# Performance work log

Hardware: AMD Instinct MI355X
Metric: run time of the kernel (lower is better)

The kernel has to match this reference:

```python
import jax, jax.numpy as jnp
import numpy as np

N_GRID = 16      # reservoir_n
CHANNELS = 4
R = 2            # receptive-field radius -> 5x5 kernel
T_STEPS = 8
NEG_SLOPE = 0.1


def _extract_patches(S):
    # S: [b, C, n, n] -> patches [b, C, 5, 5, n, n] (kernel offsets u,v)
    Sp = jnp.pad(S, ((0, 0), (0, 0), (R, R), (R, R)))
    k = 2 * R + 1
    rows = [jnp.stack([Sp[:, :, du:du + N_GRID, dv:dv + N_GRID] for dv in range(k)], axis=2)
            for du in range(k)]
    return jnp.stack(rows, axis=2)  # [b, C, k, k, n, n]


def _reservoir_step(S, W):
    # W: [n, n, C_out, C_in, k, k]; per-pixel unique weights (locally connected)
    patches = _extract_patches(S)                       # [b, c, u, v, y, x]
    out = jnp.einsum('bcuvyx,yxocuv->boyx', patches, W)  # [b, C, n, n]
    return jnp.where(out > 0, out, NEG_SLOPE * out)      # leaky_relu(0.1)


def setup_inputs() -> dict:
    key = jax.random.key(0)
    k1, k2 = jax.random.split(key)
    x = jax.random.normal(k1, (8192, 784), dtype=jnp.float32)
    # scale weights down so the T-step recurrence stays numerically tame
    W = jax.random.normal(k2, (N_GRID, N_GRID, CHANNELS, CHANNELS, 2 * R + 1, 2 * R + 1),
                          dtype=jnp.float32) * 0.05
    return {"x": x, "W": W}


def reference(x, W):
    batch = x.shape[0]
    total = N_GRID * N_GRID * CHANNELS  # 1024
    padded = jnp.pad(x, ((0, 0), (0, total - x.shape[1])))
    S = padded.reshape(batch, CHANNELS, N_GRID, N_GRID)
    for _ in range(T_STEPS):
        S = _reservoir_step(S, W)
    S_pooled = S.mean(axis=1)                 # pool over channels -> [b, n, n]
    return S_pooled.reshape(batch, -1)        # [b, n*n]
```

## Files before the change

kernel.cpp:

```cpp
#include <hip/hip_runtime.h>

#define NG 16
#define NC 4
#define BPB 8
#define TSTEPS 8
#define PITCH 34
#define CROW (NG * PITCH)

__device__ __forceinline__ void fma8(float w, const float4& s0, const float4& s1,
                                     float4& a0, float4& a1) {
    a0.x = fmaf(w, s0.x, a0.x);
    a0.y = fmaf(w, s0.y, a0.y);
    a0.z = fmaf(w, s0.z, a0.z);
    a0.w = fmaf(w, s0.w, a0.w);
    a1.x = fmaf(w, s1.x, a1.x);
    a1.y = fmaf(w, s1.y, a1.y);
    a1.z = fmaf(w, s1.z, a1.z);
    a1.w = fmaf(w, s1.w, a1.w);
}

__device__ __forceinline__ float4 lrelu4(float4 v) {
    float4 r;
    r.x = v.x > 0.f ? v.x : 0.1f * v.x;
    r.y = v.y > 0.f ? v.y : 0.1f * v.y;
    r.z = v.z > 0.f ? v.z : 0.1f * v.z;
    r.w = v.w > 0.f ? v.w : 0.1f * v.w;
    return r;
}

__global__ void wt_transpose(const float* __restrict__ W, float4* __restrict__ Wt) {
    int t = blockIdx.x * 256 + threadIdx.x;
    if (t >= 25600) return;
    int r = t >> 8;
    int pix = t & 255;
    int c = r / 25, uv = r - c * 25, u = uv / 5, v = uv - u * 5;
    int y = pix >> 4, x = pix & 15;
    float4 w = make_float4(0.f, 0.f, 0.f, 0.f);
    if ((unsigned)(y + u - 2) < 16u && (unsigned)(x + v - 2) < 16u) {
        int base = pix * 400 + c * 25 + uv;
        w.x = W[base];
        w.y = W[base + 100];
        w.z = W[base + 200];
        w.w = W[base + 300];
    }
    Wt[r * 256 + pix] = w;
}

__global__ __launch_bounds__(256, 4)
void reservoir_kernel(const float* __restrict__ X, const float4* __restrict__ Wt,
                      float* __restrict__ out, int batch) {
    __shared__ float4 smv[NC * CROW];
    float* smf = reinterpret_cast<float*>(smv);

    const int tid = threadIdx.x;
    const int y = tid >> 4;
    const int x = tid & 15;
    const long itemBase = (long)blockIdx.x * BPB;

    const float4* Wp = Wt + tid;

    float4 b0_0, b0_1, b0_2, b0_3, b0_4;
    float4 b1_0, b1_1, b1_2, b1_3, b1_4;

#define LOADBUF(B, OFF) \
    B##_0 = Wp[(OFF)]; \
    B##_1 = Wp[(OFF) + 256]; \
    B##_2 = Wp[(OFF) + 512]; \
    B##_3 = Wp[(OFF) + 768]; \
    B##_4 = Wp[(OFF) + 1024];

    LOADBUF(b0, 0)

    for (int b = 0; b < BPB; ++b) {
        long item = itemBase + b;
        const float* xr = X + item * 784;
        const int g = b >> 2, j = b & 3;
        #pragma unroll
        for (int kk = 0; kk < 4; ++kk) {
            int idx = tid + kk * 256;
            float v = 0.f;
            if (idx < 784 && item < batch) v = __builtin_nontemporal_load(&xr[idx]);
            int c = idx >> 8, rem = idx & 255, yy = rem >> 4, xx = rem & 15;
            int phys = g ^ ((xx >> 2) & 1);
            smf[((c * NG + yy) * PITCH + xx * 2 + phys) * 4 + j] = v;
        }
    }

    int ybf[5], xbf[5];
    #pragma unroll
    for (int u = 0; u < 5; ++u) {
        int yy = y + u - 2;
        yy = yy < 0 ? 0 : (yy > 15 ? 15 : yy);
        ybf[u] = yy * PITCH;
    }
    #pragma unroll
    for (int v = 0; v < 5; ++v) {
        int xv = x + v - 2;
        xv = xv < 0 ? 0 : (xv > 15 ? 15 : xv);
        xbf[v] = xv * 2 + ((xv >> 2) & 1);
    }
    const int swx = (x >> 2) & 1;
    const int pa = y * PITCH + x * 2;

    __syncthreads();

#define FMA_V(WV, V) { \
    const int i0 = sbase + xbf[V]; \
    const float4 s0 = smv[i0]; \
    const float4 s1 = smv[i0 ^ 1]; \
    fma8(WV.x, s0, s1, a00, a01); \
    fma8(WV.y, s0, s1, a10, a11); \
    fma8(WV.z, s0, s1, a20, a21); \
    fma8(WV.w, s0, s1, a30, a31); }

#define FMA5(B) FMA_V(B##_0, 0) FMA_V(B##_1, 1) FMA_V(B##_2, 2) FMA_V(B##_3, 3) FMA_V(B##_4, 4)

#define CH_A(CB, U, POFF) \
    LOADBUF(b1, POFF) \
    { const int sbase = (CB) + ybf[U]; FMA5(b0) }
#define CH_B(CB, U, POFF) \
    LOADBUF(b0, POFF) \
    { const int sbase = (CB) + ybf[U]; FMA5(b1) }

    #pragma unroll 1
    for (int t = 0; t < TSTEPS; ++t) {
        float4 a00 = {0,0,0,0}, a01 = {0,0,0,0};
        float4 a10 = {0,0,0,0}, a11 = {0,0,0,0};
        float4 a20 = {0,0,0,0}, a21 = {0,0,0,0};
        float4 a30 = {0,0,0,0}, a31 = {0,0,0,0};

        #pragma unroll 1
        for (int g = 0; g < 4; g += 2) {
            const int cb0 = g * CROW;
            const int cb1 = cb0 + CROW;
            const int wo = g * 6400;
            const int wlast = (g == 2) ? 0 : wo + 12800;

            CH_A(cb0, 0, wo + 1280)
            CH_B(cb0, 1, wo + 2560)
            CH_A(cb0, 2, wo + 3840)
            CH_B(cb0, 3, wo + 5120)
            CH_A(cb0, 4, wo + 6400)
            CH_B(cb1, 0, wo + 7680)
            CH_A(cb1, 1, wo + 8960)
            CH_B(cb1, 2, wo + 10240)
            CH_A(cb1, 3, wo + 11520)
            CH_B(cb1, 4, wlast)
        }

        a00 = lrelu4(a00); a01 = lrelu4(a01);
        a10 = lrelu4(a10); a11 = lrelu4(a11);
        a20 = lrelu4(a20); a21 = lrelu4(a21);
        a30 = lrelu4(a30); a31 = lrelu4(a31);

        if (t < TSTEPS - 1) {
            __syncthreads();
            int c0 = 0 * CROW + pa;
            smv[c0 + swx] = a00; smv[c0 + (swx ^ 1)] = a01;
            int c1 = 1 * CROW + pa;
            smv[c1 + swx] = a10; smv[c1 + (swx ^ 1)] = a11;
            int c2 = 2 * CROW + pa;
            smv[c2 + swx] = a20; smv[c2 + (swx ^ 1)] = a21;
            int c3 = 3 * CROW + pa;
            smv[c3 + swx] = a30; smv[c3 + (swx ^ 1)] = a31;
            __syncthreads();
        } else {
            float4 p0, p1;
            p0.x = (a00.x + a10.x + a20.x + a30.x) * 0.25f;
            p0.y = (a00.y + a10.y + a20.y + a30.y) * 0.25f;
            p0.z = (a00.z + a10.z + a20.z + a30.z) * 0.25f;
            p0.w = (a00.w + a10.w + a20.w + a30.w) * 0.25f;
            p1.x = (a01.x + a11.x + a21.x + a31.x) * 0.25f;
            p1.y = (a01.y + a11.y + a21.y + a31.y) * 0.25f;
            p1.z = (a01.z + a11.z + a21.z + a31.z) * 0.25f;
            p1.w = (a01.w + a11.w + a21.w + a31.w) * 0.25f;
            long ob = itemBase * 256 + tid;
            if (itemBase + 0 < batch) __builtin_nontemporal_store(p0.x, &out[ob + 0 * 256]);
            if (itemBase + 1 < batch) __builtin_nontemporal_store(p0.y, &out[ob + 1 * 256]);
            if (itemBase + 2 < batch) __builtin_nontemporal_store(p0.z, &out[ob + 2 * 256]);
            if (itemBase + 3 < batch) __builtin_nontemporal_store(p0.w, &out[ob + 3 * 256]);
            if (itemBase + 4 < batch) __builtin_nontemporal_store(p1.x, &out[ob + 4 * 256]);
            if (itemBase + 5 < batch) __builtin_nontemporal_store(p1.y, &out[ob + 5 * 256]);
            if (itemBase + 6 < batch) __builtin_nontemporal_store(p1.z, &out[ob + 6 * 256]);
            if (itemBase + 7 < batch) __builtin_nontemporal_store(p1.w, &out[ob + 7 * 256]);
        }
    }
}

extern "C" void kernel_launch(void* const* d_in, const int* in_sizes, int n_in,
                              void* d_out, int out_size, void* d_ws, size_t ws_size,
                              hipStream_t stream) {
    const float* X = (const float*)d_in[0];
    const float* W = (const float*)d_in[1];
    float* out = (float*)d_out;
    const int batch = in_sizes[0] / 784;
    const int blocks = (batch + BPB - 1) / BPB;

    wt_transpose<<<100, 256, 0, stream>>>(W, (float4*)d_ws);
    reservoir_kernel<<<blocks, 256, 0, stream>>>(
        X, (const float4*)d_ws, out, batch);
}
```

Measured before the change: 257.5 us.

## Replace horizontal LDS neighbor loads with DPP cross-lane row shifts

Each thread now loads only its own column from shared memory per kernel row. It obtains the x±1 and x±2 neighbor values via DPP row shifts within each 16-lane row, which cuts LDS reads per row from five pairs to one. Out-of-row lanes get zero through bound_ctrl, matching the zeroed boundary weights. Leaky ReLU becomes an fmax form and a waves_per_eu attribute is added. Extra DPP moves may add VALU work if they are not folded into the FMAs.

```diff
diff --git a/kernel.cpp b/kernel.cpp
--- a/kernel.cpp
+++ b/kernel.cpp
@@ -21,10 +21,25 @@
 
 __device__ __forceinline__ float4 lrelu4(float4 v) {
     float4 r;
-    r.x = v.x > 0.f ? v.x : 0.1f * v.x;
-    r.y = v.y > 0.f ? v.y : 0.1f * v.y;
-    r.z = v.z > 0.f ? v.z : 0.1f * v.z;
-    r.w = v.w > 0.f ? v.w : 0.1f * v.w;
+    r.x = fmaxf(v.x, 0.1f * v.x);
+    r.y = fmaxf(v.y, 0.1f * v.y);
+    r.z = fmaxf(v.z, 0.1f * v.z);
+    r.w = fmaxf(v.w, 0.1f * v.w);
+    return r;
+}
+
+template<int CTRL>
+__device__ __forceinline__ float dppf(float x) {
+    return __int_as_float(__builtin_amdgcn_update_dpp(
+        0, __float_as_int(x), CTRL, 0xF, 0xF, true));
+}
+template<int CTRL>
+__device__ __forceinline__ float4 dpp4(float4 v) {
+    float4 r;
+    r.x = dppf<CTRL>(v.x);
+    r.y = dppf<CTRL>(v.y);
+    r.z = dppf<CTRL>(v.z);
+    r.w = dppf<CTRL>(v.w);
     return r;
 }
 
@@ -47,6 +62,7 @@
 }
 
 __global__ __launch_bounds__(256, 4)
+__attribute__((amdgpu_waves_per_eu(4, 4)))
 void reservoir_kernel(const float* __restrict__ X, const float4* __restrict__ Wt,
                       float* __restrict__ out, int batch) {
     __shared__ float4 smv[NC * CROW];
@@ -86,41 +102,54 @@
         }
     }
 
-    int ybf[5], xbf[5];
+    int ybf[5];
     #pragma unroll
     for (int u = 0; u < 5; ++u) {
         int yy = y + u - 2;
         yy = yy < 0 ? 0 : (yy > 15 ? 15 : yy);
         ybf[u] = yy * PITCH;
     }
-    #pragma unroll
-    for (int v = 0; v < 5; ++v) {
-        int xv = x + v - 2;
-        xv = xv < 0 ? 0 : (xv > 15 ? 15 : xv);
-        xbf[v] = xv * 2 + ((xv >> 2) & 1);
-    }
     const int swx = (x >> 2) & 1;
+    const int xown = x * 2 + swx;
     const int pa = y * PITCH + x * 2;
 
     __syncthreads();
 
-#define FMA_V(WV, V) { \
-    const int i0 = sbase + xbf[V]; \
+#define CHUNK_DPP(B, CB, U) { \
+    const int i0 = (CB) + ybf[U] + xown; \
     const float4 s0 = smv[i0]; \
     const float4 s1 = smv[i0 ^ 1]; \
-    fma8(WV.x, s0, s1, a00, a01); \
-    fma8(WV.y, s0, s1, a10, a11); \
-    fma8(WV.z, s0, s1, a20, a21); \
-    fma8(WV.w, s0, s1, a30, a31); }
-
-#define FMA5(B) FMA_V(B##_0, 0) FMA_V(B##_1, 1) FMA_V(B##_2, 2) FMA_V(B##_3, 3) FMA_V(B##_4, 4)
+    fma8(B##_2.x, s0, s1, a00, a01); \
+    fma8(B##_2.y, s0, s1, a10, a11); \
+    fma8(B##_2.z, s0, s1, a20, a21); \
+    fma8(B##_2.w, s0, s1, a30, a31); \
+    { const float4 t0 = dpp4<0x111>(s0), t1 = dpp4<0x111>(s1); \
+      fma8(B##_1.x, t0, t1, a00, a01); \
+      fma8(B##_1.y, t0, t1, a10, a11); \
+      fma8(B##_1.z, t0, t1, a20, a21); \
+      fma8(B##_1.w, t0, t1, a30, a31); } \
+    { const float4 t0 = dpp4<0x101>(s0), t1 = dpp4<0x101>(s1); \
+      fma8(B##_3.x, t0, t1, a00, a01); \
+      fma8(B##_3.y, t0, t1, a10, a11); \
+      fma8(B##_3.z, t0, t1, a20, a21); \
+      fma8(B##_3.w, t0, t1, a30, a31); } \
+    { const float4 t0 = dpp4<0x112>(s0), t1 = dpp4<0x112>(s1); \
+      fma8(B##_0.x, t0, t1, a00, a01); \
+      fma8(B##_0.y, t0, t1, a10, a11); \
+      fma8(B##_0.z, t0, t1, a20, a21); \
+      fma8(B##_0.w, t0, t1, a30, a31); } \
+    { const float4 t0 = dpp4<0x102>(s0), t1 = dpp4<0x102>(s1); \
+      fma8(B##_4.x, t0, t1, a00, a01); \
+      fma8(B##_4.y, t0, t1, a10, a11); \
+      fma8(B##_4.z, t0, t1, a20, a21); \
+      fma8(B##_4.w, t0, t1, a30, a31); } }
 
 #define CH_A(CB, U, POFF) \
     LOADBUF(b1, POFF) \
-    { const int sbase = (CB) + ybf[U]; FMA5(b0) }
+    CHUNK_DPP(b0, CB, U)
 #define CH_B(CB, U, POFF) \
     LOADBUF(b0, POFF) \
-    { const int sbase = (CB) + ybf[U]; FMA5(b1) }
+    CHUNK_DPP(b1, CB, U)
 
     #pragma unroll 1
     for (int t = 0; t < TSTEPS; ++t) {
```

Measured after the change: 235.8 us. 8.4% less time.
